# Performance work log

Hardware: AMD Instinct MI355X
Metric: run time of the kernel (lower is better)

The kernel has to match this reference:

```python
import jax, jax.numpy as jnp
import numpy as np

B, N, D, H, F = 16, 512, 768, 12, 3072
HD = D // H
EPS = 1e-5
NEG_INF = -1e30  # stand-in for -inf; softmax of all -inf rows handled via nan_to_num semantics


def layer_norm(x, g, b):
    mu = jnp.mean(x, axis=-1, keepdims=True)
    var = jnp.mean(jnp.square(x - mu), axis=-1, keepdims=True)
    return (x - mu) * jax.lax.rsqrt(var + EPS) * g + b


def setup_inputs() -> dict:
    key = jax.random.key(0)
    ks = jax.random.split(key, 16)
    s = 0.02
    return {
        "x": jax.random.normal(ks[0], (B, N, D), jnp.float32),
        "spatial_encoding": jax.random.normal(ks[1], (B, N, N), jnp.float32),
        "edge_encoding": jax.random.normal(ks[2], (B, N, N), jnp.float32),
        "Wq": jax.random.normal(ks[3], (D, D), jnp.float32) * s,
        "Wk": jax.random.normal(ks[4], (D, D), jnp.float32) * s,
        "Wv": jax.random.normal(ks[5], (D, D), jnp.float32) * s,
        "bv": jnp.zeros((D,), jnp.float32),
        "Wo": jax.random.normal(ks[6], (D, D), jnp.float32) * s,
        "bo": jnp.zeros((D,), jnp.float32),
        "g1": jnp.ones((D,), jnp.float32),
        "be1": jnp.zeros((D,), jnp.float32),
        "g2": jnp.ones((D,), jnp.float32),
        "be2": jnp.zeros((D,), jnp.float32),
        "W1": jax.random.normal(ks[7], (D, F), jnp.float32) * s,
        "bf1": jnp.zeros((F,), jnp.float32),
        "W2": jax.random.normal(ks[8], (F, D), jnp.float32) * s,
        "bf2": jnp.zeros((D,), jnp.float32),
    }


def reference(x, spatial_encoding, edge_encoding, Wq, Wk, Wv, bv, Wo, bo,
              g1, be1, g2, be2, W1, bf1, W2, bf2):
    scale = D ** (-0.5)
    h = layer_norm(x, g1, be1)                              # n1(x)
    bias = (spatial_encoding + edge_encoding)[:, None]      # [B,1,N,N]

    q = (h @ Wq).reshape(B, N, H, HD).transpose(0, 2, 1, 3)  # [B,H,N,hd]
    k = (h @ Wk).reshape(B, N, H, HD).transpose(0, 2, 1, 3)
    v = (h @ Wv + bv).reshape(B, N, H, HD).transpose(0, 2, 1, 3)

    a = jnp.einsum('bhqd,bhkd->bhqk', q, k) * scale + bias   # [B,H,N,N]
    # pad rows (all-zero score rows) get -inf -> softmax NaN -> nan_to_num -> 0
    row_nonzero = jnp.any(a != 0, axis=-1, keepdims=True)
    a = jnp.where(row_nonzero, a, NEG_INF)
    p = jax.nn.softmax(a, axis=-1)
    p = jnp.where(row_nonzero, p, 0.0)  # mirrors nan_to_num on all -inf rows

    o = jnp.einsum('bhqk,bhkd->bhqd', p, v)                  # [B,H,N,hd]
    o = o.transpose(0, 2, 1, 3).reshape(B, N, D)
    att_output = o @ Wo + bo + x                              # residual

    pad_mask = jnp.any(att_output == 0, axis=-1)              # [B,N]
    ffn_in = layer_norm(x, g2, be2)                           # note: n2(x), as in source
    hmid = jax.nn.gelu(ffn_in @ W1 + bf1, approximate=True)
    ffn_out = hmid @ W2 + bf2 + att_output
    return jnp.where(pad_mask[..., None], 0.0, ffn_out)
```

## Files before the change

kernel.cpp:

```cpp
#include <hip/hip_runtime.h>
#include <math.h>

typedef unsigned short u16;
typedef __bf16 bf16x8 __attribute__((ext_vector_type(8)));
typedef float f32x4 __attribute__((ext_vector_type(4)));

__device__ __forceinline__ u16 f2bf(float f){
  union{float f; unsigned u;} v; v.f = f;
  return (u16)((v.u + 0x7fffu + ((v.u >> 16) & 1u)) >> 16);
}

#define LOG2E 1.4426950408889634f

__global__ void tpose_cast(u16* __restrict__ dst, const float* __restrict__ src,
                           int R, int C, float scale){
  __shared__ float t[32][33];
  int c0 = blockIdx.x * 32, r0 = blockIdx.y * 32;
  int tx = threadIdx.x, ty = threadIdx.y;
  #pragma unroll
  for (int i = 0; i < 4; i++)
    t[ty + i*8][tx] = src[(size_t)(r0 + ty + i*8) * C + c0 + tx];
  __syncthreads();
  #pragma unroll
  for (int i = 0; i < 4; i++)
    dst[(size_t)(c0 + ty + i*8) * R + r0 + tx] = f2bf(t[tx][ty + i*8] * scale);
}

__global__ void bias_prep(u16* __restrict__ dst, const float* __restrict__ sp,
                          const float* __restrict__ ed){
  int t = blockIdx.x * blockDim.x + threadIdx.x;
  int row = t >> 7, c0 = (t & 127) * 4;
  size_t base = (size_t)row * 512;
  float4 s = *(const float4*)&sp[base + c0];
  float4 e = *(const float4*)&ed[base + c0];
  int kt = c0 >> 7, cw = c0 & 127, fk = cw >> 4, l0 = cw & 15;
  u16* o = dst + base + kt*128 + fk;
  o[(l0+0)*8] = f2bf((s.x+e.x)*LOG2E);
  o[(l0+1)*8] = f2bf((s.y+e.y)*LOG2E);
  o[(l0+2)*8] = f2bf((s.z+e.z)*LOG2E);
  o[(l0+3)*8] = f2bf((s.w+e.w)*LOG2E);
}

__global__ void build_qkvb(float* __restrict__ qkvb, const float* __restrict__ bv){
  int i = blockIdx.x * blockDim.x + threadIdx.x;
  if (i < 2304) qkvb[i] = (i < 1536) ? 0.f : bv[i - 1536];
}

__global__ __launch_bounds__(256) void ln_kernel(
    const float* __restrict__ x,
    const float* __restrict__ g1, const float* __restrict__ be1,
    const float* __restrict__ g2, const float* __restrict__ be2,
    u16* __restrict__ h1, u16* __restrict__ h2){
  const int lane = threadIdx.x & 63, wave = threadIdx.x >> 6;
  const int row = blockIdx.x * 4 + wave;
  const float4* xr = (const float4*)(x + (size_t)row * 768);
  float4 v[3];
  float sum = 0.f, sq = 0.f;
  #pragma unroll
  for (int c = 0; c < 3; c++){
    v[c] = xr[lane + 64*c];
    sum += v[c].x + v[c].y + v[c].z + v[c].w;
    sq  += v[c].x*v[c].x + v[c].y*v[c].y + v[c].z*v[c].z + v[c].w*v[c].w;
  }
  #pragma unroll
  for (int d = 1; d < 64; d <<= 1){ sum += __shfl_xor(sum, d); sq += __shfl_xor(sq, d); }
  float mu  = sum * (1.f/768.f);
  float var = sq * (1.f/768.f) - mu*mu;
  float rs  = rsqrtf(var + 1e-5f);
  #pragma unroll
  for (int c = 0; c < 3; c++){
    int f4 = lane + 64*c;
    float4 ga = ((const float4*)g1)[f4], ba = ((const float4*)be1)[f4];
    float4 gb = ((const float4*)g2)[f4], bb = ((const float4*)be2)[f4];
    float nx = (v[c].x-mu)*rs, ny = (v[c].y-mu)*rs, nz = (v[c].z-mu)*rs, nw = (v[c].w-mu)*rs;
    ushort4 o1{f2bf(nx*ga.x+ba.x), f2bf(ny*ga.y+ba.y), f2bf(nz*ga.z+ba.z), f2bf(nw*ga.w+ba.w)};
    ushort4 o2{f2bf(nx*gb.x+bb.x), f2bf(ny*gb.y+bb.y), f2bf(nz*gb.z+bb.z), f2bf(nw*gb.w+bb.w)};
    ((ushort4*)(h1 + (size_t)row*768))[f4] = o1;
    ((ushort4*)(h2 + (size_t)row*768))[f4] = o2;
  }
}

template<int EPI>
__global__ __launch_bounds__(256, 2) void gemm_bt(
    const u16* __restrict__ A, const u16* __restrict__ Bt, void* __restrict__ Cout,
    const float* __restrict__ bias, const float* __restrict__ resid,
    int M, int Nn, int K){
  __shared__ __align__(16) u16 As[128*64];
  __shared__ __align__(16) u16 Bs[128*64];
  const int tid = threadIdx.x, lane = tid & 63, wave = tid >> 6;
  const int wm = wave >> 1, wn = wave & 1;
  const int l15 = lane & 15, lg = lane >> 4;
  const int bid = blockIdx.y * gridDim.x + blockIdx.x;
  const int cpx = (gridDim.x * gridDim.y) >> 3;
  const int swz = (bid & 7) * cpx + (bid >> 3);
  const int m0 = (swz / gridDim.x) * 128, n0 = (swz % gridDim.x) * 128;
  f32x4 acc[4][4] = {};
  for (int k0 = 0; k0 < K; k0 += 64){
    #pragma unroll
    for (int i = 0; i < 4; i++){
      int chunk = i*256 + tid;
      int row = chunk >> 3, seg = (chunk & 7) ^ (row & 7);
      __builtin_amdgcn_global_load_lds(
        (const __attribute__((address_space(1))) void*)&A[(size_t)(m0+row)*K + k0 + seg*8],
        (__attribute__((address_space(3))) void*)&As[(size_t)(i*256 + wave*64)*8],
        16, 0, 0);
      __builtin_amdgcn_global_load_lds(
        (const __attribute__((address_space(1))) void*)&Bt[(size_t)(n0+row)*K + k0 + seg*8],
        (__attribute__((address_space(3))) void*)&Bs[(size_t)(i*256 + wave*64)*8],
        16, 0, 0);
    }
    __syncthreads();
    bf16x8 af[4][2], bfr[4][2];
    #pragma unroll
    for (int i = 0; i < 4; i++){
      int ra = wm*64 + i*16 + l15, rb = wn*64 + i*16 + l15;
      #pragma unroll
      for (int kk = 0; kk < 2; kk++){
        af[i][kk]  = *(const bf16x8*)&As[ra*64 + (((kk*4 + lg) ^ (l15 & 7)) << 3)];
        bfr[i][kk] = *(const bf16x8*)&Bs[rb*64 + (((kk*4 + lg) ^ (l15 & 7)) << 3)];
      }
    }
    #pragma unroll
    for (int kk = 0; kk < 2; kk++)
      #pragma unroll
      for (int i = 0; i < 4; i++)
        #pragma unroll
        for (int j = 0; j < 4; j++)
          acc[i][j] = __builtin_amdgcn_mfma_f32_16x16x32_bf16(af[i][kk], bfr[j][kk], acc[i][j], 0, 0, 0);
    __syncthreads();
  }
  #pragma unroll
  for (int i = 0; i < 4; i++){
    int row_base = m0 + wm*64 + i*16 + lg*4;
    #pragma unroll
    for (int j = 0; j < 4; j++){
      int col = n0 + wn*64 + j*16 + l15;
      float bb = bias ? bias[col] : 0.f;
      #pragma unroll
      for (int r = 0; r < 4; r++){
        size_t idx = (size_t)(row_base + r) * Nn + col;
        float v = acc[i][j][r] + bb;
        if (EPI == 1){
          v += resid[idx];
          ((float*)Cout)[idx] = v;
        } else if (EPI == 2){
          float u = v + 0.044715f * v * v * v;
          float e = exp2f(-2.3022182f * u);
          ((u16*)Cout)[idx] = f2bf(v * __builtin_amdgcn_rcpf(1.f + e));
        } else {
          ((u16*)Cout)[idx] = f2bf(v);
        }
      }
    }
  }
}

__global__ void vtrans(const u16* __restrict__ qkv, u16* __restrict__ VTg){
  __shared__ u16 t[32][33];
  int bh = blockIdx.z, b = bh / 12, h = bh % 12;
  int n0 = blockIdx.x * 32, hd0 = blockIdx.y * 32;
  int tx = threadIdx.x, ty = threadIdx.y;
  #pragma unroll
  for (int i = 0; i < 4; i++){
    int n = n0 + ty + i*8;
    t[ty + i*8][tx] = qkv[((size_t)(b*512 + n))*2304 + 1536 + h*64 + hd0 + tx];
  }
  __syncthreads();
  #pragma unroll
  for (int i = 0; i < 4; i++){
    int hd = hd0 + ty + i*8;
    int col = n0 + tx;
    int tile = col >> 7, within = col & 127;
    int newcol = (tile << 7) + ((((within >> 3) ^ (hd & 7)) << 3)) + (within & 7);
    VTg[((size_t)bh*64 + hd)*512 + newcol] = t[tx][ty + i*8];
  }
}

__global__ __launch_bounds__(256, 2) void attn_kernel(
    const u16* __restrict__ qkv, const u16* __restrict__ VTg,
    const u16* __restrict__ biasPb, u16* __restrict__ Og){
  __shared__ __align__(16) u16 Ks[128*64];
  __shared__ __align__(16) u16 Vs[64*128];
  __shared__ __align__(16) u16 Pl[4*32*136];
  const int tid = threadIdx.x, lane = tid & 63, wave = tid >> 6;
  const int l15 = lane & 15, lg = lane >> 4;
  const int bid = blockIdx.y * 4 + blockIdx.x;
  const int swz = (bid & 7) * 96 + (bid >> 3);
  const int bh = swz >> 2, b = bh / 12, h = bh % 12;
  const int q0 = (swz & 3) * 128 + wave * 32;
  const u16* Qb = qkv + (size_t)b * 512 * 2304 + h * 64;
  const u16* Kb = Qb + 768;
  const u16* Vbh = VTg + (size_t)bh * 64 * 512;
  u16* Pw = &Pl[wave * 32 * 136];

  bf16x8 qf[2][2];
  #pragma unroll
  for (int fm = 0; fm < 2; fm++)
    #pragma unroll
    for (int kk = 0; kk < 2; kk++)
      qf[fm][kk] = *(const bf16x8*)&Qb[(size_t)(q0 + fm*16 + l15)*2304 + kk*32 + lg*8];

  f32x4 O[2][4] = {};
  float lrow[2][4] = {};

  for (int kt = 0; kt < 4; kt++){
    const int k0 = kt * 128;
    bf16x8 bb[2][4];
    #pragma unroll
    for (int fm = 0; fm < 2; fm++)
      #pragma unroll
      for (int r = 0; r < 4; r++){
        int qrow = q0 + fm*16 + lg*4 + r;
        bb[fm][r] = *(const bf16x8*)&biasPb[((size_t)(b*512 + qrow)*4 + kt)*128 + l15*8];
      }
    #pragma unroll
    for (int i = 0; i < 4; i++){
      int chunk = i*256 + tid;
      int r = chunk >> 3, cc = chunk & 7;
      __builtin_amdgcn_global_load_lds(
        (const __attribute__((address_space(1))) void*)&Kb[(size_t)(k0 + r)*2304 + ((cc ^ (r & 7)) << 3)],
        (__attribute__((address_space(3))) void*)&Ks[(size_t)(i*256 + wave*64)*8],
        16, 0, 0);
    }
    #pragma unroll
    for (int i = 0; i < 4; i++){
      int chunk = i*256 + tid;
      int r = chunk >> 4, cc = chunk & 15;
      __builtin_amdgcn_global_load_lds(
        (const __attribute__((address_space(1))) void*)&Vbh[(size_t)r*512 + k0 + (cc << 3)],
        (__attribute__((address_space(3))) void*)&Vs[(size_t)(i*256 + wave*64)*8],
        16, 0, 0);
    }
    __syncthreads();

    f32x4 S[2][8] = {};
    #pragma unroll
    for (int fk = 0; fk < 8; fk++)
      #pragma unroll
      for (int kk = 0; kk < 2; kk++){
        int row = fk*16 + l15;
        bf16x8 kf = *(const bf16x8*)&Ks[row*64 + (((kk*4 + lg) ^ (l15 & 7)) << 3)];
        S[0][fk] = __builtin_amdgcn_mfma_f32_16x16x32_bf16(qf[0][kk], kf, S[0][fk], 0,0,0);
        S[1][fk] = __builtin_amdgcn_mfma_f32_16x16x32_bf16(qf[1][kk], kf, S[1][fk], 0,0,0);
      }
    #pragma unroll
    for (int fm = 0; fm < 2; fm++)
      #pragma unroll
      for (int r = 0; r < 4; r++){
        float rs = 0.f;
        #pragma unroll
        for (int fk = 0; fk < 8; fk++){
          float p = exp2f(S[fm][fk][r] + (float)bb[fm][r][fk]);
          S[fm][fk][r] = p;
          rs += p;
        }
        rs += __shfl_xor(rs, 1); rs += __shfl_xor(rs, 2);
        rs += __shfl_xor(rs, 4); rs += __shfl_xor(rs, 8);
        lrow[fm][r] += rs;
      }
    #pragma unroll
    for (int fm = 0; fm < 2; fm++)
      #pragma unroll
      for (int fk = 0; fk < 8; fk++)
        #pragma unroll
        for (int r = 0; r < 4; r++)
          Pw[(fm*16 + lg*4 + r)*136 + fk*16 + l15] = f2bf(S[fm][fk][r]);
    bf16x8 pf[2][4];
    #pragma unroll
    for (int fm = 0; fm < 2; fm++)
      #pragma unroll
      for (int kk = 0; kk < 4; kk++)
        pf[fm][kk] = *(const bf16x8*)&Pw[(fm*16 + l15)*136 + kk*32 + lg*8];
    #pragma unroll
    for (int fn = 0; fn < 4; fn++)
      #pragma unroll
      for (int kk = 0; kk < 4; kk++){
        int row = fn*16 + l15;
        bf16x8 vf = *(const bf16x8*)&Vs[row*128 + (((kk*4 + lg) ^ (l15 & 7)) << 3)];
        O[0][fn] = __builtin_amdgcn_mfma_f32_16x16x32_bf16(pf[0][kk], vf, O[0][fn], 0,0,0);
        O[1][fn] = __builtin_amdgcn_mfma_f32_16x16x32_bf16(pf[1][kk], vf, O[1][fn], 0,0,0);
      }
    __syncthreads();
  }
  #pragma unroll
  for (int fm = 0; fm < 2; fm++)
    #pragma unroll
    for (int r = 0; r < 4; r++){
      float inv = __builtin_amdgcn_rcpf(lrow[fm][r]);
      int qrow = q0 + fm*16 + lg*4 + r;
      #pragma unroll
      for (int fn = 0; fn < 4; fn++)
        Og[((size_t)b*512 + qrow)*768 + h*64 + fn*16 + l15] = f2bf(O[fm][fn][r] * inv);
    }
}

extern "C" void kernel_launch(void* const* d_in, const int* in_sizes, int n_in,
                              void* d_out, int out_size, void* d_ws, size_t ws_size,
                              hipStream_t stream){
  const float* x   = (const float*)d_in[0];
  const float* sp  = (const float*)d_in[1];
  const float* ed  = (const float*)d_in[2];
  const float* Wq  = (const float*)d_in[3];
  const float* Wk  = (const float*)d_in[4];
  const float* Wv  = (const float*)d_in[5];
  const float* bv  = (const float*)d_in[6];
  const float* Wo  = (const float*)d_in[7];
  const float* bo  = (const float*)d_in[8];
  const float* g1  = (const float*)d_in[9];
  const float* be1 = (const float*)d_in[10];
  const float* g2  = (const float*)d_in[11];
  const float* be2 = (const float*)d_in[12];
  const float* W1  = (const float*)d_in[13];
  const float* bf1 = (const float*)d_in[14];
  const float* W2  = (const float*)d_in[15];
  const float* bf2 = (const float*)d_in[16];

  char* w = (char*)d_ws;
  size_t off = 0;
  auto alloc = [&](size_t bytes)->void*{ void* p = w + off; off += (bytes + 255) & ~(size_t)255; return p; };
  u16*   Gg    = (u16*)  alloc(8192ull*3072*2);
  u16*   qkv   = Gg;
  u16*   VTg   = (u16*)  alloc(8192ull*768*2);
  u16*   h1    = (u16*)  alloc(8192ull*768*2);
  u16*   h2    = (u16*)  alloc(8192ull*768*2);
  u16*   Og    = (u16*)  alloc(8192ull*768*2);
  float* att   = (float*)alloc(8192ull*768*4);
  u16*   biasPb= (u16*)  alloc(16ull*512*512*2);
  u16*   WqkvT = (u16*)  alloc(2304ull*768*2);
  u16*   WoT   = (u16*)  alloc(768ull*768*2);
  u16*   W1T   = (u16*)  alloc(3072ull*768*2);
  u16*   W2T   = (u16*)  alloc(768ull*3072*2);
  float* qkvb  = (float*)alloc(2304ull*4);

  const float qscale = 0.03608439182435161f * LOG2E;

  tpose_cast<<<dim3(24,24),dim3(32,8),0,stream>>>(WqkvT,            Wq, 768, 768, qscale);
  tpose_cast<<<dim3(24,24),dim3(32,8),0,stream>>>(WqkvT + 768*768,  Wk, 768, 768, 1.f);
  tpose_cast<<<dim3(24,24),dim3(32,8),0,stream>>>(WqkvT + 1536*768, Wv, 768, 768, 1.f);
  tpose_cast<<<dim3(24,24),dim3(32,8),0,stream>>>(WoT,              Wo, 768, 768, 1.f);
  tpose_cast<<<dim3(96,24),dim3(32,8),0,stream>>>(W1T, W1, 768, 3072, 1.f);
  tpose_cast<<<dim3(24,96),dim3(32,8),0,stream>>>(W2T, W2, 3072, 768, 1.f);
  bias_prep<<<4096,256,0,stream>>>(biasPb, sp, ed);
  build_qkvb<<<9,256,0,stream>>>(qkvb, bv);

  ln_kernel<<<2048,256,0,stream>>>(x, g1, be1, g2, be2, h1, h2);

  gemm_bt<0><<<dim3(18,64),256,0,stream>>>(h1, WqkvT, qkv, qkvb, nullptr, 8192, 2304, 768);
  vtrans<<<dim3(16,2,192),dim3(32,8),0,stream>>>(qkv, VTg);

  attn_kernel<<<dim3(4,192),256,0,stream>>>(qkv, VTg, biasPb, Og);

  gemm_bt<1><<<dim3(6,64),256,0,stream>>>(Og, WoT, att, bo, x, 8192, 768, 768);

  gemm_bt<2><<<dim3(24,64),256,0,stream>>>(h2, W1T, Gg, bf1, nullptr, 8192, 3072, 768);
  gemm_bt<1><<<dim3(6,64),256,0,stream>>>(Gg, W2T, (float*)d_out, bf2, att, 8192, 768, 3072);
}
```

Measured before the change: 263.6 us.

## Double-buffer GEMM LDS tiles and store attention residual in bf16

The GEMM kernel now uses two LDS buffers per operand and issues the next K-tile's async global-to-LDS loads before computing on the current tile. This is meant to overlap memory latency with MFMA work and drops the trailing barrier. The attention-output intermediate (Wo projection plus residual) is now written as bf16 and read back as bf16 in the final FFN GEMM, halving that traffic. The costs are doubled LDS use per block, which may limit occupancy, and reduced precision on the residual path.

```diff
diff --git a/kernel.cpp b/kernel.cpp
--- a/kernel.cpp
+++ b/kernel.cpp
@@ -8,6 +8,9 @@
 __device__ __forceinline__ u16 f2bf(float f){
   union{float f; unsigned u;} v; v.f = f;
   return (u16)((v.u + 0x7fffu + ((v.u >> 16) & 1u)) >> 16);
+}
+__device__ __forceinline__ float bf2f(u16 b){
+  union{unsigned u; float f;} v; v.u = (unsigned)b << 16; return v.f;
 }
 
 #define LOG2E 1.4426950408889634f
@@ -83,10 +86,10 @@
 template<int EPI>
 __global__ __launch_bounds__(256, 2) void gemm_bt(
     const u16* __restrict__ A, const u16* __restrict__ Bt, void* __restrict__ Cout,
-    const float* __restrict__ bias, const float* __restrict__ resid,
+    const float* __restrict__ bias, const void* __restrict__ resid,
     int M, int Nn, int K){
-  __shared__ __align__(16) u16 As[128*64];
-  __shared__ __align__(16) u16 Bs[128*64];
+  __shared__ __align__(16) u16 As[2][128*64];
+  __shared__ __align__(16) u16 Bs[2][128*64];
   const int tid = threadIdx.x, lane = tid & 63, wave = tid >> 6;
   const int wm = wave >> 1, wn = wave & 1;
   const int l15 = lane & 15, lg = lane >> 4;
@@ -94,30 +97,37 @@
   const int cpx = (gridDim.x * gridDim.y) >> 3;
   const int swz = (bid & 7) * cpx + (bid >> 3);
   const int m0 = (swz / gridDim.x) * 128, n0 = (swz % gridDim.x) * 128;
+
+#define STAGE(buf, k0) do { \
+    _Pragma("unroll") \
+    for (int i_ = 0; i_ < 4; i_++){ \
+      int chunk_ = i_*256 + tid; \
+      int row_ = chunk_ >> 3, seg_ = (chunk_ & 7) ^ (row_ & 7); \
+      __builtin_amdgcn_global_load_lds( \
+        (const __attribute__((address_space(1))) void*)&A[(size_t)(m0+row_)*K + (k0) + seg_*8], \
+        (__attribute__((address_space(3))) void*)&As[buf][(size_t)(i_*256 + wave*64)*8], 16, 0, 0); \
+      __builtin_amdgcn_global_load_lds( \
+        (const __attribute__((address_space(1))) void*)&Bt[(size_t)(n0+row_)*K + (k0) + seg_*8], \
+        (__attribute__((address_space(3))) void*)&Bs[buf][(size_t)(i_*256 + wave*64)*8], 16, 0, 0); \
+    } } while(0)
+
   f32x4 acc[4][4] = {};
-  for (int k0 = 0; k0 < K; k0 += 64){
-    #pragma unroll
-    for (int i = 0; i < 4; i++){
-      int chunk = i*256 + tid;
-      int row = chunk >> 3, seg = (chunk & 7) ^ (row & 7);
-      __builtin_amdgcn_global_load_lds(
-        (const __attribute__((address_space(1))) void*)&A[(size_t)(m0+row)*K + k0 + seg*8],
-        (__attribute__((address_space(3))) void*)&As[(size_t)(i*256 + wave*64)*8],
-        16, 0, 0);
-      __builtin_amdgcn_global_load_lds(
-        (const __attribute__((address_space(1))) void*)&Bt[(size_t)(n0+row)*K + k0 + seg*8],
-        (__attribute__((address_space(3))) void*)&Bs[(size_t)(i*256 + wave*64)*8],
-        16, 0, 0);
-    }
+  const int nt = K >> 6;
+  STAGE(0, 0);
+  int cur = 0;
+  for (int t = 0; t < nt; t++){
     __syncthreads();
+    if (t + 1 < nt) STAGE(cur ^ 1, (t+1) << 6);
+    const u16* Ac = As[cur];
+    const u16* Bc = Bs[cur];
     bf16x8 af[4][2], bfr[4][2];
     #pragma unroll
     for (int i = 0; i < 4; i++){
       int ra = wm*64 + i*16 + l15, rb = wn*64 + i*16 + l15;
       #pragma unroll
       for (int kk = 0; kk < 2; kk++){
-        af[i][kk]  = *(const bf16x8*)&As[ra*64 + (((kk*4 + lg) ^ (l15 & 7)) << 3)];
-        bfr[i][kk] = *(const bf16x8*)&Bs[rb*64 + (((kk*4 + lg) ^ (l15 & 7)) << 3)];
+        af[i][kk]  = *(const bf16x8*)&Ac[ra*64 + (((kk*4 + lg) ^ (l15 & 7)) << 3)];
+        bfr[i][kk] = *(const bf16x8*)&Bc[rb*64 + (((kk*4 + lg) ^ (l15 & 7)) << 3)];
       }
     }
     #pragma unroll
@@ -127,8 +137,9 @@
         #pragma unroll
         for (int j = 0; j < 4; j++)
           acc[i][j] = __builtin_amdgcn_mfma_f32_16x16x32_bf16(af[i][kk], bfr[j][kk], acc[i][j], 0, 0, 0);
-    __syncthreads();
-  }
+    cur ^= 1;
+  }
+#undef STAGE
   #pragma unroll
   for (int i = 0; i < 4; i++){
     int row_base = m0 + wm*64 + i*16 + lg*4;
@@ -140,8 +151,11 @@
       for (int r = 0; r < 4; r++){
         size_t idx = (size_t)(row_base + r) * Nn + col;
         float v = acc[i][j][r] + bb;
-        if (EPI == 1){
-          v += resid[idx];
+        if (EPI == 3){
+          v += ((const float*)resid)[idx];
+          ((u16*)Cout)[idx] = f2bf(v);
+        } else if (EPI == 4){
+          v += bf2f(((const u16*)resid)[idx]);
           ((float*)Cout)[idx] = v;
         } else if (EPI == 2){
           float u = v + 0.044715f * v * v * v;
@@ -324,7 +338,7 @@
   u16*   h1    = (u16*)  alloc(8192ull*768*2);
   u16*   h2    = (u16*)  alloc(8192ull*768*2);
   u16*   Og    = (u16*)  alloc(8192ull*768*2);
-  float* att   = (float*)alloc(8192ull*768*4);
+  u16*   attb  = (u16*)  alloc(8192ull*768*2);
   u16*   biasPb= (u16*)  alloc(16ull*512*512*2);
   u16*   WqkvT = (u16*)  alloc(2304ull*768*2);
   u16*   WoT   = (u16*)  alloc(768ull*768*2);
@@ -350,8 +364,8 @@
 
   attn_kernel<<<dim3(4,192),256,0,stream>>>(qkv, VTg, biasPb, Og);
 
-  gemm_bt<1><<<dim3(6,64),256,0,stream>>>(Og, WoT, att, bo, x, 8192, 768, 768);
+  gemm_bt<3><<<dim3(6,64),256,0,stream>>>(Og, WoT, attb, bo, x, 8192, 768, 768);
 
   gemm_bt<2><<<dim3(24,64),256,0,stream>>>(h2, W1T, Gg, bf1, nullptr, 8192, 3072, 768);
-  gemm_bt<1><<<dim3(6,64),256,0,stream>>>(Gg, W2T, (float*)d_out, bf2, att, 8192, 768, 3072);
-}
+  gemm_bt<4><<<dim3(6,64),256,0,stream>>>(Gg, W2T, (float*)d_out, bf2, attb, 8192, 768, 3072);
+}
```

Measured after the change: 282.9 us. +7.4%, slower.

## Use 256x128 GEMM tiles for QKV and FFN1, store attention residual in bf16

Applied to the files above, without the earlier changes.

Adds a second GEMM kernel with 256-row tiles, which doubles A-tile reuse per B-tile load. It is used for the QKV projection and the first FFN GEMM. The attention-output residual buffer is now written and read as bf16 instead of fp32, which halves that traffic. The larger tile raises register and LDS pressure, and the bf16 residual lowers precision of the skip path.

```diff
diff --git a/kernel.cpp b/kernel.cpp
--- a/kernel.cpp
+++ b/kernel.cpp
@@ -8,6 +8,9 @@
 __device__ __forceinline__ u16 f2bf(float f){
   union{float f; unsigned u;} v; v.f = f;
   return (u16)((v.u + 0x7fffu + ((v.u >> 16) & 1u)) >> 16);
+}
+__device__ __forceinline__ float bf2f(u16 b){
+  union{unsigned u; float f;} v; v.u = (unsigned)b << 16; return v.f;
 }
 
 #define LOG2E 1.4426950408889634f
@@ -83,7 +86,7 @@
 template<int EPI>
 __global__ __launch_bounds__(256, 2) void gemm_bt(
     const u16* __restrict__ A, const u16* __restrict__ Bt, void* __restrict__ Cout,
-    const float* __restrict__ bias, const float* __restrict__ resid,
+    const float* __restrict__ bias, const void* __restrict__ resid,
     int M, int Nn, int K){
   __shared__ __align__(16) u16 As[128*64];
   __shared__ __align__(16) u16 Bs[128*64];
@@ -102,12 +105,10 @@
       int row = chunk >> 3, seg = (chunk & 7) ^ (row & 7);
       __builtin_amdgcn_global_load_lds(
         (const __attribute__((address_space(1))) void*)&A[(size_t)(m0+row)*K + k0 + seg*8],
-        (__attribute__((address_space(3))) void*)&As[(size_t)(i*256 + wave*64)*8],
-        16, 0, 0);
+        (__attribute__((address_space(3))) void*)&As[(size_t)(i*256 + wave*64)*8], 16, 0, 0);
       __builtin_amdgcn_global_load_lds(
         (const __attribute__((address_space(1))) void*)&Bt[(size_t)(n0+row)*K + k0 + seg*8],
-        (__attribute__((address_space(3))) void*)&Bs[(size_t)(i*256 + wave*64)*8],
-        16, 0, 0);
+        (__attribute__((address_space(3))) void*)&Bs[(size_t)(i*256 + wave*64)*8], 16, 0, 0);
     }
     __syncthreads();
     bf16x8 af[4][2], bfr[4][2];
@@ -140,10 +141,87 @@
       for (int r = 0; r < 4; r++){
         size_t idx = (size_t)(row_base + r) * Nn + col;
         float v = acc[i][j][r] + bb;
-        if (EPI == 1){
-          v += resid[idx];
+        if (EPI == 3){
+          v += ((const float*)resid)[idx];
+          ((u16*)Cout)[idx] = f2bf(v);
+        } else if (EPI == 4){
+          v += bf2f(((const u16*)resid)[idx]);
           ((float*)Cout)[idx] = v;
-        } else if (EPI == 2){
+        } else {
+          ((u16*)Cout)[idx] = f2bf(v);
+        }
+      }
+    }
+  }
+}
+
+template<int EPI>
+__global__ __launch_bounds__(256, 2) void gemm_bt2(
+    const u16* __restrict__ A, const u16* __restrict__ Bt, void* __restrict__ Cout,
+    const float* __restrict__ bias,
+    int M, int Nn, int K){
+  __shared__ __align__(16) u16 As[256*64];
+  __shared__ __align__(16) u16 Bs[128*64];
+  const int tid = threadIdx.x, lane = tid & 63, wave = tid >> 6;
+  const int wm = wave >> 1, wn = wave & 1;
+  const int l15 = lane & 15, lg = lane >> 4;
+  const int bid = blockIdx.y * gridDim.x + blockIdx.x;
+  const int cpx = (gridDim.x * gridDim.y) >> 3;
+  const int swz = (bid & 7) * cpx + (bid >> 3);
+  const int m0 = (swz / gridDim.x) * 256, n0 = (swz % gridDim.x) * 128;
+
+  f32x4 acc[8][4] = {};
+  for (int k0 = 0; k0 < K; k0 += 64){
+    #pragma unroll
+    for (int i = 0; i < 8; i++){
+      int chunk = i*256 + tid;
+      int row = chunk >> 3, seg = (chunk & 7) ^ (row & 7);
+      __builtin_amdgcn_global_load_lds(
+        (const __attribute__((address_space(1))) void*)&A[(size_t)(m0+row)*K + k0 + seg*8],
+        (__attribute__((address_space(3))) void*)&As[(size_t)(i*256 + wave*64)*8], 16, 0, 0);
+    }
+    #pragma unroll
+    for (int i = 0; i < 4; i++){
+      int chunk = i*256 + tid;
+      int row = chunk >> 3, seg = (chunk & 7) ^ (row & 7);
+      __builtin_amdgcn_global_load_lds(
+        (const __attribute__((address_space(1))) void*)&Bt[(size_t)(n0+row)*K + k0 + seg*8],
+        (__attribute__((address_space(3))) void*)&Bs[(size_t)(i*256 + wave*64)*8], 16, 0, 0);
+    }
+    __syncthreads();
+    bf16x8 bfr[4][2];
+    #pragma unroll
+    for (int j = 0; j < 4; j++){
+      int rb = wn*64 + j*16 + l15;
+      #pragma unroll
+      for (int kk = 0; kk < 2; kk++)
+        bfr[j][kk] = *(const bf16x8*)&Bs[rb*64 + (((kk*4 + lg) ^ (l15 & 7)) << 3)];
+    }
+    #pragma unroll
+    for (int i = 0; i < 8; i++){
+      int ra = wm*128 + i*16 + l15;
+      bf16x8 af0 = *(const bf16x8*)&As[ra*64 + (((0*4 + lg) ^ (l15 & 7)) << 3)];
+      bf16x8 af1 = *(const bf16x8*)&As[ra*64 + (((1*4 + lg) ^ (l15 & 7)) << 3)];
+      #pragma unroll
+      for (int j = 0; j < 4; j++){
+        acc[i][j] = __builtin_amdgcn_mfma_f32_16x16x32_bf16(af0, bfr[j][0], acc[i][j], 0, 0, 0);
+        acc[i][j] = __builtin_amdgcn_mfma_f32_16x16x32_bf16(af1, bfr[j][1], acc[i][j], 0, 0, 0);
+      }
+    }
+    __syncthreads();
+  }
+  #pragma unroll
+  for (int i = 0; i < 8; i++){
+    int row_base = m0 + wm*128 + i*16 + lg*4;
+    #pragma unroll
+    for (int j = 0; j < 4; j++){
+      int col = n0 + wn*64 + j*16 + l15;
+      float bb = bias ? bias[col] : 0.f;
+      #pragma unroll
+      for (int r = 0; r < 4; r++){
+        size_t idx = (size_t)(row_base + r) * Nn + col;
+        float v = acc[i][j][r] + bb;
+        if (EPI == 2){
           float u = v + 0.044715f * v * v * v;
           float e = exp2f(-2.3022182f * u);
           ((u16*)Cout)[idx] = f2bf(v * __builtin_amdgcn_rcpf(1.f + e));
@@ -324,7 +402,7 @@
   u16*   h1    = (u16*)  alloc(8192ull*768*2);
   u16*   h2    = (u16*)  alloc(8192ull*768*2);
   u16*   Og    = (u16*)  alloc(8192ull*768*2);
-  float* att   = (float*)alloc(8192ull*768*4);
+  u16*   attb  = (u16*)  alloc(8192ull*768*2);
   u16*   biasPb= (u16*)  alloc(16ull*512*512*2);
   u16*   WqkvT = (u16*)  alloc(2304ull*768*2);
   u16*   WoT   = (u16*)  alloc(768ull*768*2);
@@ -345,13 +423,13 @@
 
   ln_kernel<<<2048,256,0,stream>>>(x, g1, be1, g2, be2, h1, h2);
 
-  gemm_bt<0><<<dim3(18,64),256,0,stream>>>(h1, WqkvT, qkv, qkvb, nullptr, 8192, 2304, 768);
+  gemm_bt2<0><<<dim3(18,32),256,0,stream>>>(h1, WqkvT, qkv, qkvb, 8192, 2304, 768);
   vtrans<<<dim3(16,2,192),dim3(32,8),0,stream>>>(qkv, VTg);
 
   attn_kernel<<<dim3(4,192),256,0,stream>>>(qkv, VTg, biasPb, Og);
 
-  gemm_bt<1><<<dim3(6,64),256,0,stream>>>(Og, WoT, att, bo, x, 8192, 768, 768);
-
-  gemm_bt<2><<<dim3(24,64),256,0,stream>>>(h2, W1T, Gg, bf1, nullptr, 8192, 3072, 768);
-  gemm_bt<1><<<dim3(6,64),256,0,stream>>>(Gg, W2T, (float*)d_out, bf2, att, 8192, 768, 3072);
-}
+  gemm_bt<3><<<dim3(6,64),256,0,stream>>>(Og, WoT, attb, bo, x, 8192, 768, 768);
+
+  gemm_bt2<2><<<dim3(24,32),256,0,stream>>>(h2, W1T, Gg, bf1, 8192, 3072, 768);
+  gemm_bt<4><<<dim3(6,64),256,0,stream>>>(Gg, W2T, (float*)d_out, bf2, attb, 8192, 768, 3072);
+}
```

New measurement: 282.6 us. +7.2%, slower.

## Fold layernorm affine into weights and store attention residual in bf16

Applied to the files above, without the earlier changes.

The layernorm gamma is folded into the transposed QKV and W1 weights, and beta into precomputed GEMM biases (new fold_bias kernel). This lets one shared normalized activation feed both branches instead of writing two. The attention output plus residual is now stored as bf16 rather than fp32, which halves that intermediate's write and read traffic. The six transpose launches are merged into one kernel. Risks: the bf16 residual loses precision in the final output, and fold_bias is a serial 768-step dot product per column running on few blocks.

```diff
diff --git a/kernel.cpp b/kernel.cpp
--- a/kernel.cpp
+++ b/kernel.cpp
@@ -9,21 +9,58 @@
   union{float f; unsigned u;} v; v.f = f;
   return (u16)((v.u + 0x7fffu + ((v.u >> 16) & 1u)) >> 16);
 }
+__device__ __forceinline__ float bf2f(u16 b){
+  union{unsigned u; float f;} v; v.u = (unsigned)b << 16; return v.f;
+}
 
 #define LOG2E 1.4426950408889634f
 
-__global__ void tpose_cast(u16* __restrict__ dst, const float* __restrict__ src,
-                           int R, int C, float scale){
+__global__ void prep_weights(const float* __restrict__ Wq, const float* __restrict__ Wk,
+                             const float* __restrict__ Wv, const float* __restrict__ Wo,
+                             const float* __restrict__ W1, const float* __restrict__ W2,
+                             const float* __restrict__ g1, const float* __restrict__ g2,
+                             u16* __restrict__ WqkvT, u16* __restrict__ WoT,
+                             u16* __restrict__ W1T, u16* __restrict__ W2T, float qscale){
   __shared__ float t[32][33];
-  int c0 = blockIdx.x * 32, r0 = blockIdx.y * 32;
+  int bid = blockIdx.x;
+  const float* src; u16* dst; const float* rs; float sc; int R, C, bx, by;
+  if (bid < 576)      {            src=Wq; dst=WqkvT;          rs=g1;      sc=qscale; R=768;  C=768;  bx=bid%24; by=bid/24; }
+  else if (bid <1152) { bid-=576;  src=Wk; dst=WqkvT+768*768;  rs=g1;      sc=1.f;    R=768;  C=768;  bx=bid%24; by=bid/24; }
+  else if (bid <1728) { bid-=1152; src=Wv; dst=WqkvT+1536*768; rs=g1;      sc=1.f;    R=768;  C=768;  bx=bid%24; by=bid/24; }
+  else if (bid <2304) { bid-=1728; src=Wo; dst=WoT;            rs=nullptr; sc=1.f;    R=768;  C=768;  bx=bid%24; by=bid/24; }
+  else if (bid <4608) { bid-=2304; src=W1; dst=W1T;            rs=g2;      sc=1.f;    R=768;  C=3072; bx=bid%96; by=bid/96; }
+  else                { bid-=4608; src=W2; dst=W2T;            rs=nullptr; sc=1.f;    R=3072; C=768;  bx=bid%24; by=bid/24; }
+  int c0 = bx * 32, r0 = by * 32;
   int tx = threadIdx.x, ty = threadIdx.y;
   #pragma unroll
   for (int i = 0; i < 4; i++)
     t[ty + i*8][tx] = src[(size_t)(r0 + ty + i*8) * C + c0 + tx];
   __syncthreads();
+  float fac = (rs ? rs[r0 + tx] : 1.f) * sc;
   #pragma unroll
   for (int i = 0; i < 4; i++)
-    dst[(size_t)(c0 + ty + i*8) * R + r0 + tx] = f2bf(t[tx][ty + i*8] * scale);
+    dst[(size_t)(c0 + ty + i*8) * R + r0 + tx] = f2bf(t[tx][ty + i*8] * fac);
+}
+
+__global__ void fold_bias(const float* __restrict__ Wq, const float* __restrict__ Wk,
+                          const float* __restrict__ Wv, const float* __restrict__ W1,
+                          const float* __restrict__ be1, const float* __restrict__ be2,
+                          const float* __restrict__ bv, const float* __restrict__ bf1,
+                          float* __restrict__ qkvb, float* __restrict__ bf1f){
+  int j = blockIdx.x * 256 + threadIdx.x;
+  if (j < 2304){
+    const float* W; int col; float s;
+    if (j < 768)       { W = Wq; col = j;        s = 0.f; }
+    else if (j < 1536) { W = Wk; col = j - 768;  s = 0.f; }
+    else               { W = Wv; col = j - 1536; s = bv[col]; }
+    for (int k = 0; k < 768; k++) s += be1[k] * W[(size_t)k*768 + col];
+    qkvb[j] = s;
+  } else if (j < 5376){
+    int col = j - 2304;
+    float s = bf1[col];
+    for (int k = 0; k < 768; k++) s += be2[k] * W1[(size_t)k*3072 + col];
+    bf1f[col] = s;
+  }
 }
 
 __global__ void bias_prep(u16* __restrict__ dst, const float* __restrict__ sp,
@@ -41,16 +78,8 @@
   o[(l0+3)*8] = f2bf((s.w+e.w)*LOG2E);
 }
 
-__global__ void build_qkvb(float* __restrict__ qkvb, const float* __restrict__ bv){
-  int i = blockIdx.x * blockDim.x + threadIdx.x;
-  if (i < 2304) qkvb[i] = (i < 1536) ? 0.f : bv[i - 1536];
-}
-
 __global__ __launch_bounds__(256) void ln_kernel(
-    const float* __restrict__ x,
-    const float* __restrict__ g1, const float* __restrict__ be1,
-    const float* __restrict__ g2, const float* __restrict__ be2,
-    u16* __restrict__ h1, u16* __restrict__ h2){
+    const float* __restrict__ x, u16* __restrict__ hn){
   const int lane = threadIdx.x & 63, wave = threadIdx.x >> 6;
   const int row = blockIdx.x * 4 + wave;
   const float4* xr = (const float4*)(x + (size_t)row * 768);
@@ -70,20 +99,16 @@
   #pragma unroll
   for (int c = 0; c < 3; c++){
     int f4 = lane + 64*c;
-    float4 ga = ((const float4*)g1)[f4], ba = ((const float4*)be1)[f4];
-    float4 gb = ((const float4*)g2)[f4], bb = ((const float4*)be2)[f4];
-    float nx = (v[c].x-mu)*rs, ny = (v[c].y-mu)*rs, nz = (v[c].z-mu)*rs, nw = (v[c].w-mu)*rs;
-    ushort4 o1{f2bf(nx*ga.x+ba.x), f2bf(ny*ga.y+ba.y), f2bf(nz*ga.z+ba.z), f2bf(nw*ga.w+ba.w)};
-    ushort4 o2{f2bf(nx*gb.x+bb.x), f2bf(ny*gb.y+bb.y), f2bf(nz*gb.z+bb.z), f2bf(nw*gb.w+bb.w)};
-    ((ushort4*)(h1 + (size_t)row*768))[f4] = o1;
-    ((ushort4*)(h2 + (size_t)row*768))[f4] = o2;
+    ushort4 o{f2bf((v[c].x-mu)*rs), f2bf((v[c].y-mu)*rs),
+              f2bf((v[c].z-mu)*rs), f2bf((v[c].w-mu)*rs)};
+    ((ushort4*)(hn + (size_t)row*768))[f4] = o;
   }
 }
 
 template<int EPI>
 __global__ __launch_bounds__(256, 2) void gemm_bt(
     const u16* __restrict__ A, const u16* __restrict__ Bt, void* __restrict__ Cout,
-    const float* __restrict__ bias, const float* __restrict__ resid,
+    const float* __restrict__ bias, const void* __restrict__ resid,
     int M, int Nn, int K){
   __shared__ __align__(16) u16 As[128*64];
   __shared__ __align__(16) u16 Bs[128*64];
@@ -102,12 +127,10 @@
       int row = chunk >> 3, seg = (chunk & 7) ^ (row & 7);
       __builtin_amdgcn_global_load_lds(
         (const __attribute__((address_space(1))) void*)&A[(size_t)(m0+row)*K + k0 + seg*8],
-        (__attribute__((address_space(3))) void*)&As[(size_t)(i*256 + wave*64)*8],
-        16, 0, 0);
+        (__attribute__((address_space(3))) void*)&As[(size_t)(i*256 + wave*64)*8], 16, 0, 0);
       __builtin_amdgcn_global_load_lds(
         (const __attribute__((address_space(1))) void*)&Bt[(size_t)(n0+row)*K + k0 + seg*8],
-        (__attribute__((address_space(3))) void*)&Bs[(size_t)(i*256 + wave*64)*8],
-        16, 0, 0);
+        (__attribute__((address_space(3))) void*)&Bs[(size_t)(i*256 + wave*64)*8], 16, 0, 0);
     }
     __syncthreads();
     bf16x8 af[4][2], bfr[4][2];
@@ -140,8 +163,11 @@
       for (int r = 0; r < 4; r++){
         size_t idx = (size_t)(row_base + r) * Nn + col;
         float v = acc[i][j][r] + bb;
-        if (EPI == 1){
-          v += resid[idx];
+        if (EPI == 3){
+          v += ((const float*)resid)[idx];
+          ((u16*)Cout)[idx] = f2bf(v);
+        } else if (EPI == 4){
+          v += bf2f(((const u16*)resid)[idx]);
           ((float*)Cout)[idx] = v;
         } else if (EPI == 2){
           float u = v + 0.044715f * v * v * v;
@@ -321,37 +347,33 @@
   u16*   Gg    = (u16*)  alloc(8192ull*3072*2);
   u16*   qkv   = Gg;
   u16*   VTg   = (u16*)  alloc(8192ull*768*2);
-  u16*   h1    = (u16*)  alloc(8192ull*768*2);
-  u16*   h2    = (u16*)  alloc(8192ull*768*2);
+  u16*   hn    = (u16*)  alloc(8192ull*768*2);
   u16*   Og    = (u16*)  alloc(8192ull*768*2);
-  float* att   = (float*)alloc(8192ull*768*4);
+  u16*   attb  = (u16*)  alloc(8192ull*768*2);
   u16*   biasPb= (u16*)  alloc(16ull*512*512*2);
   u16*   WqkvT = (u16*)  alloc(2304ull*768*2);
   u16*   WoT   = (u16*)  alloc(768ull*768*2);
   u16*   W1T   = (u16*)  alloc(3072ull*768*2);
   u16*   W2T   = (u16*)  alloc(768ull*3072*2);
   float* qkvb  = (float*)alloc(2304ull*4);
+  float* bf1f  = (float*)alloc(3072ull*4);
 
   const float qscale = 0.03608439182435161f * LOG2E;
 
-  tpose_cast<<<dim3(24,24),dim3(32,8),0,stream>>>(WqkvT,            Wq, 768, 768, qscale);
-  tpose_cast<<<dim3(24,24),dim3(32,8),0,stream>>>(WqkvT + 768*768,  Wk, 768, 768, 1.f);
-  tpose_cast<<<dim3(24,24),dim3(32,8),0,stream>>>(WqkvT + 1536*768, Wv, 768, 768, 1.f);
-  tpose_cast<<<dim3(24,24),dim3(32,8),0,stream>>>(WoT,              Wo, 768, 768, 1.f);
-  tpose_cast<<<dim3(96,24),dim3(32,8),0,stream>>>(W1T, W1, 768, 3072, 1.f);
-  tpose_cast<<<dim3(24,96),dim3(32,8),0,stream>>>(W2T, W2, 3072, 768, 1.f);
-  bias_prep<<<4096,256,0,stream>>>(biasPb, sp, ed);
-  build_qkvb<<<9,256,0,stream>>>(qkvb, bv);
-
-  ln_kernel<<<2048,256,0,stream>>>(x, g1, be1, g2, be2, h1, h2);
-
-  gemm_bt<0><<<dim3(18,64),256,0,stream>>>(h1, WqkvT, qkv, qkvb, nullptr, 8192, 2304, 768);
+  prep_weights<<<6912, dim3(32,8), 0, stream>>>(Wq, Wk, Wv, Wo, W1, W2, g1, g2,
+                                                WqkvT, WoT, W1T, W2T, qscale);
+  fold_bias<<<21, 256, 0, stream>>>(Wq, Wk, Wv, W1, be1, be2, bv, bf1, qkvb, bf1f);
+  bias_prep<<<4096, 256, 0, stream>>>(biasPb, sp, ed);
+
+  ln_kernel<<<2048, 256, 0, stream>>>(x, hn);
+
+  gemm_bt<0><<<dim3(18,64),256,0,stream>>>(hn, WqkvT, qkv, qkvb, nullptr, 8192, 2304, 768);
   vtrans<<<dim3(16,2,192),dim3(32,8),0,stream>>>(qkv, VTg);
 
   attn_kernel<<<dim3(4,192),256,0,stream>>>(qkv, VTg, biasPb, Og);
 
-  gemm_bt<1><<<dim3(6,64),256,0,stream>>>(Og, WoT, att, bo, x, 8192, 768, 768);
-
-  gemm_bt<2><<<dim3(24,64),256,0,stream>>>(h2, W1T, Gg, bf1, nullptr, 8192, 3072, 768);
-  gemm_bt<1><<<dim3(6,64),256,0,stream>>>(Gg, W2T, (float*)d_out, bf2, att, 8192, 768, 3072);
-}
+  gemm_bt<3><<<dim3(6,64),256,0,stream>>>(Og, WoT, attb, bo, x, 8192, 768, 768);
+
+  gemm_bt<2><<<dim3(24,64),256,0,stream>>>(hn, W1T, Gg, bf1f, nullptr, 8192, 3072, 768);
+  gemm_bt<4><<<dim3(6,64),256,0,stream>>>(Gg, W2T, (float*)d_out, bf2, attb, 8192, 768, 3072);
+}
```

Measured after the change: 293.8 us. 11.5% more time.
